# Performance work log

Measured on AMD Instinct MI355X. Metric: run time of the kernel, lower is better.

The kernel has to match this reference:

```python
import jax, jax.numpy as jnp
import numpy as np

NMUL = 1
NEARZERO = 1e-5
ROUTING_LEN = 15
N_DYN = 3
N_STATIC = 13  # layout includes parRT, parAC (present in STATIC_PARAM_NAMES but unused in the step)


def _descale(x, lb, ub):
    return lb + x * (ub - lb)


def setup_inputs() -> dict:
    key = jax.random.key(0)
    k1, k2, k3 = jax.random.split(key, 3)
    T, G = 365, 50000
    u = jax.random.uniform(k1, (T, G, 3), dtype=jnp.float32)
    prcp = u[..., 0] * 10.0                 # mm/day
    tmean = (u[..., 1] - 0.3) * 20.0        # degC, roughly [-6, 14] so snow branch is exercised
    pet = u[..., 2] * 5.0                   # mm/day
    forcing = jnp.stack([prcp, tmean, pet], axis=-1)
    dyn_raw = jax.random.uniform(k2, (T, G, N_DYN * NMUL), dtype=jnp.float32)
    static_raw = jax.random.uniform(k3, (G, N_STATIC * NMUL + 2), dtype=jnp.float32)
    return {"forcing": forcing, "dyn_raw": dyn_raw, "static_raw": static_raw}


def _hbv_forward(forcing, dyn_raw, static_raw):
    T, G, _ = forcing.shape
    dt = forcing.dtype
    # --- descale dynamic params (per-timestep): parBETA, parK0, parBETAET ---
    dyn = dyn_raw.reshape(T, G, N_DYN, NMUL)
    parBETA = _descale(dyn[:, :, 0], 1.0, 6.0)
    parK0 = _descale(dyn[:, :, 1], 0.05, 0.9)
    parBETAET = _descale(dyn[:, :, 2], 0.3, 5.0)
    # --- descale static params ---
    st = static_raw[:, :N_STATIC * NMUL].reshape(G, N_STATIC, NMUL)
    parFC = _descale(st[:, 0], 50.0, 1000.0)
    parK1 = _descale(st[:, 1], 0.01, 0.5)
    parK2 = _descale(st[:, 2], 0.001, 0.2)
    parLP = _descale(st[:, 3], 0.2, 1.0)
    parPERC = _descale(st[:, 4], 0.0, 10.0)
    parUZL = _descale(st[:, 5], 0.0, 100.0)
    parTT = _descale(st[:, 6], -2.5, 2.5)
    parCFMAX = _descale(st[:, 7], 0.5, 10.0)
    parCFR = _descale(st[:, 8], 0.0, 0.1)
    parCWH = _descale(st[:, 9], 0.0, 0.2)
    parC = _descale(st[:, 10], 0.0, 1.0)
    rout = static_raw[:, N_STATIC * NMUL:]
    rout_a = _descale(rout[:, 0], 0.0, 2.9)
    rout_b = _descale(rout[:, 1], 0.0, 6.5)

    Pm = jnp.broadcast_to(forcing[..., 0:1], (T, G, NMUL))
    Tm = jnp.broadcast_to(forcing[..., 1:2], (T, G, NMUL))
    PETm = jnp.broadcast_to(forcing[..., 2:3], (T, G, NMUL))

    def step(carry, xs):
        SNOWPACK, MELTWATER, SM, SUZ, SLZ = carry
        PRECIP, TEMP, PET, pBETA, pK0, pBETAET = xs
        is_rain = (TEMP >= parTT).astype(dt)
        RAIN = PRECIP * is_rain
        SNOW = PRECIP * (1.0 - is_rain)
        SNOWPACK = SNOWPACK + SNOW
        melt = jnp.minimum(jnp.maximum(parCFMAX * (TEMP - parTT), 0.0), SNOWPACK)
        MELTWATER = MELTWATER + melt
        SNOWPACK = SNOWPACK - melt
        refreezing = jnp.minimum(jnp.maximum(parCFR * parCFMAX * (parTT - TEMP), 0.0), MELTWATER)
        SNOWPACK = SNOWPACK + refreezing
        MELTWATER = MELTWATER - refreezing
        tosoil = jnp.maximum(MELTWATER - parCWH * SNOWPACK, 0.0)
        MELTWATER = MELTWATER - tosoil
        soil_wetness = jnp.clip((SM / parFC) ** pBETA, 0.0, 1.0)
        recharge = (RAIN + tosoil) * soil_wetness
        SM = SM + RAIN + tosoil - recharge
        excess = jnp.maximum(SM - parFC, 0.0)
        SM = SM - excess
        evapfactor = jnp.clip((SM / (parLP * parFC)) ** pBETAET, 0.0, 1.0)
        ETact = jnp.minimum(SM, PET * evapfactor)
        SM = jnp.maximum(SM - ETact, NEARZERO)
        capillary = jnp.minimum(SLZ, parC * SLZ * (1.0 - jnp.minimum(SM / parFC, 1.0)))
        SM = jnp.maximum(SM + capillary, NEARZERO)
        SLZ = jnp.maximum(SLZ - capillary, NEARZERO)
        SUZ = SUZ + recharge + excess
        PERC = jnp.minimum(SUZ, parPERC)
        SUZ = SUZ - PERC
        Q0 = pK0 * jnp.maximum(SUZ - parUZL, 0.0)
        SUZ = SUZ - Q0
        Q1 = parK1 * SUZ
        SUZ = SUZ - Q1
        SLZ = jnp.maximum(SLZ + PERC, 0.0)
        Q2 = parK2 * SLZ
        SLZ = SLZ - Q2
        return (SNOWPACK, MELTWATER, SM, SUZ, SLZ), Q0 + Q1 + Q2

    init = tuple(jnp.full((G, NMUL), 0.001, dtype=dt) for _ in range(5))
    _, Qall = jax.lax.scan(step, init, (Pm, Tm, PETm, parBETA, parK0, parBETAET))
    Qsim = Qall.mean(axis=-1)  # [T, G]: average over nmul components

    # --- gamma unit-hydrograph routing (hydroDL UH_gamma + causal conv, lenF = 15) ---
    aa = jax.nn.relu(rout_a) + 0.1      # shape param, [G]
    theta = jax.nn.relu(rout_b) + 0.5   # scale param, [G]
    t = jnp.arange(0.5, ROUTING_LEN, dtype=dt)[:, None]  # [15, 1] midpoints
    w = (t ** (aa - 1.0)) * jnp.exp(-t / theta) / (jnp.exp(jax.lax.lgamma(aa)) * theta ** aa)
    w = w / w.sum(axis=0)  # [15, G], normalized UH weights
    Qpad = jnp.pad(Qsim, ((ROUTING_LEN - 1, 0), (0, 0)))
    # causal conv: Qrout[t] = sum_k w[k] * Qsim[t-k]; fixed 15-tap loop
    Qrout = sum(w[k] * jax.lax.dynamic_slice_in_dim(Qpad, ROUTING_LEN - 1 - k, T, axis=0)
                for k in range(ROUTING_LEN))
    return Qrout  # streamflow [T, G]


def reference(forcing, dyn_raw, static_raw):
    return _hbv_forward(forcing, dyn_raw, static_raw)
```

## Files before the change

kernel.cpp:

```cpp
#include <hip/hip_runtime.h>

#define NEARZERO 1e-5f
#define RLEN 15
#define LOG2E 1.4426950408889634f

struct __attribute__((packed, aligned(4))) F3 { float x, y, z; };
static __device__ __forceinline__ F3 ld3f(const float* p) {
    return *reinterpret_cast<const F3*>(p);
}

struct Par { float FC, invFC, invLPFC, K1, K2, PERC, UZL, TT, CFMAX, CFRC, CWH, C; };

template<int PH>
__device__ __forceinline__ void finish_step(
    const Par& pr, float& SUZ, float& SLZ,
    float rxP, float k0P,
    float (&acc)[RLEN], const float (&w)[RLEN],
    float& cs, float*& outp, int G, bool guard)
{
    SUZ += rxP;
    const float PERCv = fminf(SUZ, pr.PERC);
    SUZ -= PERCv;
    const float Q0 = k0P * fmaxf(SUZ - pr.UZL, 0.0f);
    SUZ -= Q0;
    const float Q1 = pr.K1 * SUZ;
    SUZ -= Q1;
    SLZ += PERCv;
    const float Q2 = pr.K2 * SLZ;
    SLZ -= Q2;
    const float Qs = Q0 + Q1 + Q2;

    const float qr = fmaf(w[0], Qs, acc[PH]);
    acc[PH] = 0.0f;
#pragma unroll
    for (int k = 1; k < RLEN; ++k) {
        const int j = (PH + k) % RLEN;
        acc[j] = fmaf(w[k], Qs, acc[j]);
    }
    if (guard) __builtin_nontemporal_store(qr, outp);
    outp += G;
    cs = pr.C * SLZ;
}

__device__ __forceinline__ void ab_step(
    const F3& f, const F3& d3, const Par& pr,
    float& SP, float& MW, float& SM, float& SLZ,
    float cs, float& rxP, float& k0P)
{
    const float pBETA   = fmaf(d3.x, 5.0f, 1.0f);
    const float pBETAET = fmaf(d3.z, 4.7f, 0.3f);

    const float dT   = f.y - pr.TT;
    const float RAIN = (dT >= 0.0f) ? f.x : 0.0f;
    SP += f.x - RAIN;
    const float melt = __builtin_amdgcn_fmed3f(pr.CFMAX * dT, 0.0f, SP);
    MW += melt;  SP -= melt;
    const float refr = __builtin_amdgcn_fmed3f(pr.CFRC * (0.0f - dT), 0.0f, MW);
    SP += refr;  MW -= refr;
    const float tosoil = fmaxf(fmaf(-pr.CWH, SP, MW), 0.0f);
    MW -= tosoil;

    const float sw = fminf(exp2f(pBETA * __log2f(SM * pr.invFC)), 1.0f);
    const float rt = RAIN + tosoil;
    const float rc = rt * sw;
    SM = fmaf(rt, 1.0f - sw, SM);
    const float ex = fmaxf(SM - pr.FC, 0.0f);
    SM = fminf(SM, pr.FC);
    const float ef = fminf(exp2f(pBETAET * __log2f(SM * pr.invLPFC)), 1.0f);
    SM = fmaxf(SM - f.z * ef, NEARZERO);
    const float cap = cs * (1.0f - fminf(SM * pr.invFC, 1.0f));
    SM  = fmaxf(SM + cap, NEARZERO);
    SLZ = fmaxf(SLZ - cap, NEARZERO);

    rxP = rc + ex;
    k0P = fmaf(d3.y, 0.85f, 0.05f);
}

__global__ __launch_bounds__(256, 1)
void hbv_kernel(const float* __restrict__ forcing,
                const float* __restrict__ dynr,
                const float* __restrict__ statr,
                float* __restrict__ out,
                int G)
{
    const int g  = blockIdx.x * 256 + threadIdx.x;
    const int gc = (g < G) ? g : (G - 1);
    const bool guard = (g < G);

    const float* sp = statr + (size_t)gc * 15;
    Par pr;
    pr.FC    = fmaf(sp[0], 950.0f, 50.0f);
    pr.K1    = fmaf(sp[1], 0.49f, 0.01f);
    pr.K2    = fmaf(sp[2], 0.199f, 0.001f);
    const float parLP = fmaf(sp[3], 0.8f, 0.2f);
    pr.PERC  = sp[4] * 10.0f;
    pr.UZL   = sp[5] * 100.0f;
    pr.TT    = fmaf(sp[6], 5.0f, -2.5f);
    pr.CFMAX = fmaf(sp[7], 9.5f, 0.5f);
    pr.CFRC  = (sp[8] * 0.1f) * pr.CFMAX;
    pr.CWH   = sp[9] * 0.2f;
    pr.C     = sp[10];
    const float rout_a = sp[13] * 2.9f;
    const float rout_b = sp[14] * 6.5f;
    pr.invFC   = 1.0f / pr.FC;
    pr.invLPFC = 1.0f / (parLP * pr.FC);

    const float aa    = fmaxf(rout_a, 0.0f) + 0.1f;
    const float theta = fmaxf(rout_b, 0.0f) + 0.5f;
    const float am1   = aa - 1.0f;
    const float nitl2 = -LOG2E / theta;
    float w[RLEN];
    float wsum = 0.0f;
#pragma unroll
    for (int k = 0; k < RLEN; ++k) {
        const float tk = (float)k + 0.5f;
        w[k] = exp2f(am1 * __log2f(tk) + tk * nitl2);
        wsum += w[k];
    }
    const float winv = 1.0f / wsum;
#pragma unroll
    for (int k = 0; k < RLEN; ++k) w[k] *= winv;

    float SP_ = 0.001f, MW = 0.001f, SM = 0.001f, SUZ = 0.001f, SLZ = 0.001f;
    float acc[RLEN];
#pragma unroll
    for (int k = 0; k < RLEN; ++k) acc[k] = 0.0f;
    float rxP = 0.0f, k0P = 0.0f, cs = 0.0f;

    const size_t sT = (size_t)G * 3;
    const float* pF = forcing + (size_t)gc * 3;
    const float* pD = dynr    + (size_t)gc * 3;
    float* outp = out + g;

    F3 bF[5], bD[5];
    bF[0] = ld3f(pF);          bD[0] = ld3f(pD);
    bF[1] = ld3f(pF + sT);     bD[1] = ld3f(pD + sT);
    bF[2] = ld3f(pF + 2 * sT); bD[2] = ld3f(pD + 2 * sT);
    bF[3] = ld3f(pF + 3 * sT); bD[3] = ld3f(pD + 3 * sT);
    bF[4] = ld3f(pF + 4 * sT); bD[4] = ld3f(pD + 4 * sT);

    const float* rF = pF + 5 * sT;
    const float* rD = pD + 5 * sT;

    cs = pr.C * SLZ;
    {
        const F3 f_ = bF[0], d_ = bD[0];
        bF[0] = ld3f(rF); bD[0] = ld3f(rD);
        rF += sT; rD += sT;
        __builtin_amdgcn_sched_barrier(0x7);
        ab_step(f_, d_, pr, SP_, MW, SM, SLZ, cs, rxP, k0P);
    }

#define ITER(MM, FP, DP) do { \
    constexpr int PH_ = (MM) % RLEN; \
    constexpr int S_  = ((MM) + 1) % 5; \
    finish_step<PH_>(pr, SUZ, SLZ, rxP, k0P, acc, w, cs, outp, G, guard); \
    const F3 f_ = bF[S_], d_ = bD[S_]; \
    bF[S_] = ld3f(FP); bD[S_] = ld3f(DP); \
    __builtin_amdgcn_sched_barrier(0x7); \
    ab_step(f_, d_, pr, SP_, MW, SM, SLZ, cs, rxP, k0P); \
} while (0)

#define ITERADV(MM) do { ITER(MM, rF, rD); rF += sT; rD += sT; } while (0)

#define ITER_NL(MM) do { \
    constexpr int PH_ = (MM) % RLEN; \
    constexpr int S_  = ((MM) + 1) % 5; \
    finish_step<PH_>(pr, SUZ, SLZ, rxP, k0P, acc, w, cs, outp, G, guard); \
    const F3 f_ = bF[S_], d_ = bD[S_]; \
    ab_step(f_, d_, pr, SP_, MW, SM, SLZ, cs, rxP, k0P); \
} while (0)

    for (int i = 0; i < 23; ++i) {
        ITERADV(0);  ITERADV(1);  ITERADV(2);  ITERADV(3);  ITERADV(4);
        ITERADV(5);  ITERADV(6);  ITERADV(7);  ITERADV(8);  ITERADV(9);
        ITERADV(10); ITERADV(11); ITERADV(12); ITERADV(13); ITERADV(14);
    }
    ITERADV(0);  ITERADV(1);  ITERADV(2);  ITERADV(3);  ITERADV(4);
    ITERADV(5);  ITERADV(6);  ITERADV(7);  ITERADV(8);  ITERADV(9);
    ITERADV(10); ITERADV(11); ITERADV(12); ITERADV(13);
    ITER(14, pF + (size_t)364 * sT, pD + (size_t)364 * sT);
    ITER_NL(0); ITER_NL(1); ITER_NL(2); ITER_NL(3);
    finish_step<4>(pr, SUZ, SLZ, rxP, k0P, acc, w, cs, outp, G, guard);
#undef ITER_NL
#undef ITERADV
#undef ITER
}

extern "C" void kernel_launch(void* const* d_in, const int* in_sizes, int n_in,
                              void* d_out, int out_size, void* d_ws, size_t ws_size,
                              hipStream_t stream) {
    const float* forcing = (const float*)d_in[0];
    const float* dynr    = (const float*)d_in[1];
    const float* statr   = (const float*)d_in[2];
    float* out = (float*)d_out;

    const int G = in_sizes[2] / 15;
    const int block = 256;
    const int grid  = (G + block - 1) / block;
    hbv_kernel<<<grid, block, 0, stream>>>(forcing, dynr, statr, out, G);
}
```

Baseline: 99.85 us.

## Process two catchments per thread with interleaved fused timestep for ILP

Each thread now simulates two independent grid cells (g and g+half), running their HBV recurrences interleaved in one fused step so the serial dependency chains can overlap. The prefetch depth drops from 5 to 3 timesteps per cell, and addressing moves to 32-bit byte offsets from a base pointer. This halves the thread count, trading thread-level parallelism for instruction-level parallelism, and roughly doubles register use. It assumes G is even, since odd G would leave the last cell uncomputed.

```diff
diff --git a/kernel.cpp b/kernel.cpp
--- a/kernel.cpp
+++ b/kernel.cpp
@@ -5,18 +5,153 @@
 #define LOG2E 1.4426950408889634f
 
 struct __attribute__((packed, aligned(4))) F3 { float x, y, z; };
-static __device__ __forceinline__ F3 ld3f(const float* p) {
-    return *reinterpret_cast<const F3*>(p);
+static __device__ __forceinline__ F3 ldo(const char* base, unsigned voff) {
+    return *reinterpret_cast<const F3*>(base + voff);
 }
 
 struct Par { float FC, invFC, invLPFC, K1, K2, PERC, UZL, TT, CFMAX, CFRC, CWH, C; };
 
+static __device__ __forceinline__ void load_par(const float* sp, Par& pr,
+                                                float& ra, float& rb) {
+    pr.FC    = fmaf(sp[0], 950.0f, 50.0f);
+    pr.K1    = fmaf(sp[1], 0.49f, 0.01f);
+    pr.K2    = fmaf(sp[2], 0.199f, 0.001f);
+    const float parLP = fmaf(sp[3], 0.8f, 0.2f);
+    pr.PERC  = sp[4] * 10.0f;
+    pr.UZL   = sp[5] * 100.0f;
+    pr.TT    = fmaf(sp[6], 5.0f, -2.5f);
+    pr.CFMAX = fmaf(sp[7], 9.5f, 0.5f);
+    pr.CFRC  = (sp[8] * 0.1f) * pr.CFMAX;
+    pr.CWH   = sp[9] * 0.2f;
+    pr.C     = sp[10];
+    ra       = sp[13] * 2.9f;
+    rb       = sp[14] * 6.5f;
+    pr.invFC   = 1.0f / pr.FC;
+    pr.invLPFC = 1.0f / (parLP * pr.FC);
+}
+
+static __device__ __forceinline__ void make_w(float ra, float rb, float (&w)[RLEN]) {
+    const float aa    = fmaxf(ra, 0.0f) + 0.1f;
+    const float theta = fmaxf(rb, 0.0f) + 0.5f;
+    const float am1   = aa - 1.0f;
+    const float nitl2 = -LOG2E / theta;
+    float wsum = 0.0f;
+#pragma unroll
+    for (int k = 0; k < RLEN; ++k) {
+        const float tk = (float)k + 0.5f;
+        w[k] = exp2f(am1 * __log2f(tk) + tk * nitl2);
+        wsum += w[k];
+    }
+    const float winv = 1.0f / wsum;
+#pragma unroll
+    for (int k = 0; k < RLEN; ++k) w[k] *= winv;
+}
+
+__device__ __forceinline__ void ab_step(
+    const F3& f, const F3& d3, const Par& pr,
+    float& SP, float& MW, float& SM, float& SLZ,
+    float cs, float& rxP, float& k0P)
+{
+    const float dT   = f.y - pr.TT;
+    const float RAIN = (dT >= 0.0f) ? f.x : 0.0f;
+    SP += f.x - RAIN;
+    const float melt = __builtin_amdgcn_fmed3f(pr.CFMAX * dT, 0.0f, SP);
+    MW += melt;  SP -= melt;
+    const float refr = __builtin_amdgcn_fmed3f(pr.CFRC * (0.0f - dT), 0.0f, MW);
+    SP += refr;  MW -= refr;
+    const float tosoil = fmaxf(fmaf(-pr.CWH, SP, MW), 0.0f);
+    MW -= tosoil;
+    const float sw = fminf(exp2f(fmaf(d3.x, 5.0f, 1.0f) * __log2f(SM * pr.invFC)), 1.0f);
+    const float rt = RAIN + tosoil;
+    const float rc = rt * sw;
+    SM = fmaf(rt, 1.0f - sw, SM);
+    const float ex = fmaxf(SM - pr.FC, 0.0f);
+    SM = fminf(SM, pr.FC);
+    const float ef = fminf(exp2f(fmaf(d3.z, 4.7f, 0.3f) * __log2f(SM * pr.invLPFC)), 1.0f);
+    SM = fmaxf(SM - f.z * ef, NEARZERO);
+    const float cap = cs * (1.0f - fminf(SM * pr.invFC, 1.0f));
+    SM  = fmaxf(SM + cap, NEARZERO);
+    SLZ = fmaxf(SLZ - cap, NEARZERO);
+    rxP = rc + ex;
+    k0P = fmaf(d3.y, 0.85f, 0.05f);
+}
+
 template<int PH>
-__device__ __forceinline__ void finish_step(
-    const Par& pr, float& SUZ, float& SLZ,
-    float rxP, float k0P,
-    float (&acc)[RLEN], const float (&w)[RLEN],
-    float& cs, float*& outp, int G, bool guard)
+__device__ __forceinline__ void fused2(
+    const F3 fA, const F3 dA, const F3 fB, const F3 dB,
+    const Par& pA, const Par& pB,
+    float& SPa, float& MWa, float& SMa, float& SUa, float& SLa,
+    float& SPb, float& MWb, float& SMb, float& SUb, float& SLb,
+    float& rxA, float& k0A, float& rxB, float& k0B,
+    float (&accA)[RLEN], float (&accB)[RLEN],
+    const float (&wA)[RLEN], const float (&wB)[RLEN],
+    float* oA, float* oB, bool guard)
+{
+    const float t1A = __log2f(SMa * pA.invFC);
+    const float t1B = __log2f(SMb * pB.invFC);
+    const float dTA = fA.y - pA.TT;               const float dTB = fB.y - pB.TT;
+    const float RNA = (dTA >= 0.0f) ? fA.x : 0.0f;
+    const float RNB = (dTB >= 0.0f) ? fB.x : 0.0f;
+    SPa += fA.x - RNA;                            SPb += fB.x - RNB;
+    const float mlA = __builtin_amdgcn_fmed3f(pA.CFMAX * dTA, 0.0f, SPa);
+    const float mlB = __builtin_amdgcn_fmed3f(pB.CFMAX * dTB, 0.0f, SPb);
+    MWa += mlA;  SPa -= mlA;                      MWb += mlB;  SPb -= mlB;
+    const float rfA = __builtin_amdgcn_fmed3f(pA.CFRC * (0.0f - dTA), 0.0f, MWa);
+    const float rfB = __builtin_amdgcn_fmed3f(pB.CFRC * (0.0f - dTB), 0.0f, MWb);
+    SPa += rfA;  MWa -= rfA;                      SPb += rfB;  MWb -= rfB;
+    const float tsA = fmaxf(fmaf(-pA.CWH, SPa, MWa), 0.0f);
+    const float tsB = fmaxf(fmaf(-pB.CWH, SPb, MWb), 0.0f);
+    MWa -= tsA;                                   MWb -= tsB;
+    SUa += rxA;                                   SUb += rxB;
+    const float PCa = fminf(SUa, pA.PERC);        const float PCb = fminf(SUb, pB.PERC);
+    SUa -= PCa;                                   SUb -= PCb;
+    const float Q0a = k0A * fmaxf(SUa - pA.UZL, 0.0f);
+    const float Q0b = k0B * fmaxf(SUb - pB.UZL, 0.0f);
+    SUa -= Q0a;                                   SUb -= Q0b;
+    const float Q1a = pA.K1 * SUa;                const float Q1b = pB.K1 * SUb;
+    SUa -= Q1a;                                   SUb -= Q1b;
+    const float swA = fminf(exp2f(fmaf(dA.x, 5.0f, 1.0f) * t1A), 1.0f);
+    const float swB = fminf(exp2f(fmaf(dB.x, 5.0f, 1.0f) * t1B), 1.0f);
+    SLa += PCa;                                   SLb += PCb;
+    const float Q2a = pA.K2 * SLa;                const float Q2b = pB.K2 * SLb;
+    SLa -= Q2a;                                   SLb -= Q2b;
+    const float Qsa = Q0a + Q1a + Q2a;            const float Qsb = Q0b + Q1b + Q2b;
+    const float csA = pA.C * SLa;                 const float csB = pB.C * SLb;
+    const float rtA = RNA + tsA;                  const float rtB = RNB + tsB;
+    const float rcA = rtA * swA;                  const float rcB = rtB * swB;
+    SMa = fmaf(rtA, 1.0f - swA, SMa);             SMb = fmaf(rtB, 1.0f - swB, SMb);
+    const float exA = fmaxf(SMa - pA.FC, 0.0f);   const float exB = fmaxf(SMb - pB.FC, 0.0f);
+    SMa = fminf(SMa, pA.FC);                      SMb = fminf(SMb, pB.FC);
+    const float t2A = __log2f(SMa * pA.invLPFC);
+    const float t2B = __log2f(SMb * pB.invLPFC);
+    const float qrA = fmaf(wA[0], Qsa, accA[PH]);
+    const float qrB = fmaf(wB[0], Qsb, accB[PH]);
+    accA[PH] = 0.0f;                              accB[PH] = 0.0f;
+#pragma unroll
+    for (int k = 1; k < RLEN; ++k) {
+        const int j = (PH + k) % RLEN;
+        accA[j] = fmaf(wA[k], Qsa, accA[j]);
+        accB[j] = fmaf(wB[k], Qsb, accB[j]);
+    }
+    if (guard) {
+        __builtin_nontemporal_store(qrA, oA);
+        __builtin_nontemporal_store(qrB, oB);
+    }
+    const float efA = fminf(exp2f(fmaf(dA.z, 4.7f, 0.3f) * t2A), 1.0f);
+    const float efB = fminf(exp2f(fmaf(dB.z, 4.7f, 0.3f) * t2B), 1.0f);
+    SMa = fmaxf(SMa - fA.z * efA, NEARZERO);      SMb = fmaxf(SMb - fB.z * efB, NEARZERO);
+    const float cpA = csA * (1.0f - fminf(SMa * pA.invFC, 1.0f));
+    const float cpB = csB * (1.0f - fminf(SMb * pB.invFC, 1.0f));
+    SMa = fmaxf(SMa + cpA, NEARZERO);             SMb = fmaxf(SMb + cpB, NEARZERO);
+    SLa = fmaxf(SLa - cpA, NEARZERO);             SLb = fmaxf(SLb - cpB, NEARZERO);
+    rxA = rcA + exA;                              rxB = rcB + exB;
+    k0A = fmaf(dA.y, 0.85f, 0.05f);               k0B = fmaf(dB.y, 0.85f, 0.05f);
+}
+
+template<int PH>
+__device__ __forceinline__ void finish_last(
+    const Par& pr, float& SUZ, float& SLZ, float rxP, float k0P,
+    float (&acc)[RLEN], const float (&w)[RLEN], float* outp, bool guard)
 {
     SUZ += rxP;
     const float PERCv = fminf(SUZ, pr.PERC);
@@ -29,51 +164,8 @@
     const float Q2 = pr.K2 * SLZ;
     SLZ -= Q2;
     const float Qs = Q0 + Q1 + Q2;
-
     const float qr = fmaf(w[0], Qs, acc[PH]);
-    acc[PH] = 0.0f;
-#pragma unroll
-    for (int k = 1; k < RLEN; ++k) {
-        const int j = (PH + k) % RLEN;
-        acc[j] = fmaf(w[k], Qs, acc[j]);
-    }
     if (guard) __builtin_nontemporal_store(qr, outp);
-    outp += G;
-    cs = pr.C * SLZ;
-}
-
-__device__ __forceinline__ void ab_step(
-    const F3& f, const F3& d3, const Par& pr,
-    float& SP, float& MW, float& SM, float& SLZ,
-    float cs, float& rxP, float& k0P)
-{
-    const float pBETA   = fmaf(d3.x, 5.0f, 1.0f);
-    const float pBETAET = fmaf(d3.z, 4.7f, 0.3f);
-
-    const float dT   = f.y - pr.TT;
-    const float RAIN = (dT >= 0.0f) ? f.x : 0.0f;
-    SP += f.x - RAIN;
-    const float melt = __builtin_amdgcn_fmed3f(pr.CFMAX * dT, 0.0f, SP);
-    MW += melt;  SP -= melt;
-    const float refr = __builtin_amdgcn_fmed3f(pr.CFRC * (0.0f - dT), 0.0f, MW);
-    SP += refr;  MW -= refr;
-    const float tosoil = fmaxf(fmaf(-pr.CWH, SP, MW), 0.0f);
-    MW -= tosoil;
-
-    const float sw = fminf(exp2f(pBETA * __log2f(SM * pr.invFC)), 1.0f);
-    const float rt = RAIN + tosoil;
-    const float rc = rt * sw;
-    SM = fmaf(rt, 1.0f - sw, SM);
-    const float ex = fmaxf(SM - pr.FC, 0.0f);
-    SM = fminf(SM, pr.FC);
-    const float ef = fminf(exp2f(pBETAET * __log2f(SM * pr.invLPFC)), 1.0f);
-    SM = fmaxf(SM - f.z * ef, NEARZERO);
-    const float cap = cs * (1.0f - fminf(SM * pr.invFC, 1.0f));
-    SM  = fmaxf(SM + cap, NEARZERO);
-    SLZ = fmaxf(SLZ - cap, NEARZERO);
-
-    rxP = rc + ex;
-    k0P = fmaf(d3.y, 0.85f, 0.05f);
 }
 
 __global__ __launch_bounds__(256, 1)
@@ -81,108 +173,85 @@
                 const float* __restrict__ dynr,
                 const float* __restrict__ statr,
                 float* __restrict__ out,
-                int G)
-{
-    const int g  = blockIdx.x * 256 + threadIdx.x;
-    const int gc = (g < G) ? g : (G - 1);
-    const bool guard = (g < G);
-
-    const float* sp = statr + (size_t)gc * 15;
-    Par pr;
-    pr.FC    = fmaf(sp[0], 950.0f, 50.0f);
-    pr.K1    = fmaf(sp[1], 0.49f, 0.01f);
-    pr.K2    = fmaf(sp[2], 0.199f, 0.001f);
-    const float parLP = fmaf(sp[3], 0.8f, 0.2f);
-    pr.PERC  = sp[4] * 10.0f;
-    pr.UZL   = sp[5] * 100.0f;
-    pr.TT    = fmaf(sp[6], 5.0f, -2.5f);
-    pr.CFMAX = fmaf(sp[7], 9.5f, 0.5f);
-    pr.CFRC  = (sp[8] * 0.1f) * pr.CFMAX;
-    pr.CWH   = sp[9] * 0.2f;
-    pr.C     = sp[10];
-    const float rout_a = sp[13] * 2.9f;
-    const float rout_b = sp[14] * 6.5f;
-    pr.invFC   = 1.0f / pr.FC;
-    pr.invLPFC = 1.0f / (parLP * pr.FC);
-
-    const float aa    = fmaxf(rout_a, 0.0f) + 0.1f;
-    const float theta = fmaxf(rout_b, 0.0f) + 0.5f;
-    const float am1   = aa - 1.0f;
-    const float nitl2 = -LOG2E / theta;
-    float w[RLEN];
-    float wsum = 0.0f;
-#pragma unroll
-    for (int k = 0; k < RLEN; ++k) {
-        const float tk = (float)k + 0.5f;
-        w[k] = exp2f(am1 * __log2f(tk) + tk * nitl2);
-        wsum += w[k];
-    }
-    const float winv = 1.0f / wsum;
-#pragma unroll
-    for (int k = 0; k < RLEN; ++k) w[k] *= winv;
-
-    float SP_ = 0.001f, MW = 0.001f, SM = 0.001f, SUZ = 0.001f, SLZ = 0.001f;
-    float acc[RLEN];
-#pragma unroll
-    for (int k = 0; k < RLEN; ++k) acc[k] = 0.0f;
-    float rxP = 0.0f, k0P = 0.0f, cs = 0.0f;
-
-    const size_t sT = (size_t)G * 3;
-    const float* pF = forcing + (size_t)gc * 3;
-    const float* pD = dynr    + (size_t)gc * 3;
-    float* outp = out + g;
-
-    F3 bF[5], bD[5];
-    bF[0] = ld3f(pF);          bD[0] = ld3f(pD);
-    bF[1] = ld3f(pF + sT);     bD[1] = ld3f(pD + sT);
-    bF[2] = ld3f(pF + 2 * sT); bD[2] = ld3f(pD + 2 * sT);
-    bF[3] = ld3f(pF + 3 * sT); bD[3] = ld3f(pD + 3 * sT);
-    bF[4] = ld3f(pF + 4 * sT); bD[4] = ld3f(pD + 4 * sT);
-
-    const float* rF = pF + 5 * sT;
-    const float* rD = pD + 5 * sT;
-
-    cs = pr.C * SLZ;
+                int G, int half)
+{
+    const int g = blockIdx.x * 256 + threadIdx.x;
+    const bool guard = (g < half);
+    const int gA = guard ? g : (half - 1);
+    const int gB = gA + half;
+
+    Par pA, pB; float raA, rbA, raB, rbB;
+    load_par(statr + (size_t)gA * 15, pA, raA, rbA);
+    load_par(statr + (size_t)gB * 15, pB, raB, rbB);
+    float wA[RLEN], wB[RLEN];
+    make_w(raA, rbA, wA);
+    make_w(raB, rbB, wB);
+
+    float SPa = 0.001f, MWa = 0.001f, SMa = 0.001f, SUa = 0.001f, SLa = 0.001f;
+    float SPb = 0.001f, MWb = 0.001f, SMb = 0.001f, SUb = 0.001f, SLb = 0.001f;
+    float accA[RLEN], accB[RLEN];
+#pragma unroll
+    for (int k = 0; k < RLEN; ++k) { accA[k] = 0.0f; accB[k] = 0.0f; }
+    float rxA = 0.0f, k0A = 0.0f, rxB = 0.0f, k0B = 0.0f;
+
+    const char* fbase = (const char*)forcing;
+    const char* dbase = (const char*)dynr;
+    char*       obase = (char*)out;
+    const unsigned G12 = (unsigned)G * 12u;
+    const unsigned G4  = (unsigned)G * 4u;
+    const unsigned HB4 = (unsigned)half * 4u;
+    unsigned vA = (unsigned)gA * 12u;
+    unsigned vB = (unsigned)gB * 12u;
+    unsigned vO = (unsigned)g * 4u;
+
+    F3 bFA[3], bDA[3], bFB[3], bDB[3];
+#pragma unroll
+    for (int r = 0; r < 3; ++r) {
+        bFA[r] = ldo(fbase, vA); bDA[r] = ldo(dbase, vA);
+        bFB[r] = ldo(fbase, vB); bDB[r] = ldo(dbase, vB);
+        vA += G12; vB += G12;
+    }
+
     {
-        const F3 f_ = bF[0], d_ = bD[0];
-        bF[0] = ld3f(rF); bD[0] = ld3f(rD);
-        rF += sT; rD += sT;
+        const float cs0A = pA.C * SLa, cs0B = pB.C * SLb;
+        const F3 fA_ = bFA[0], dA_ = bDA[0], fB_ = bFB[0], dB_ = bDB[0];
+        bFA[0] = ldo(fbase, vA); bDA[0] = ldo(dbase, vA);
+        bFB[0] = ldo(fbase, vB); bDB[0] = ldo(dbase, vB);
+        vA += G12; vB += G12;
         __builtin_amdgcn_sched_barrier(0x7);
-        ab_step(f_, d_, pr, SP_, MW, SM, SLZ, cs, rxP, k0P);
-    }
-
-#define ITER(MM, FP, DP) do { \
+        ab_step(fA_, dA_, pA, SPa, MWa, SMa, SLa, cs0A, rxA, k0A);
+        ab_step(fB_, dB_, pB, SPb, MWb, SMb, SLb, cs0B, rxB, k0B);
+    }
+
+#define ITER(MM, VLA, VLB, DOLOAD) do { \
     constexpr int PH_ = (MM) % RLEN; \
-    constexpr int S_  = ((MM) + 1) % 5; \
-    finish_step<PH_>(pr, SUZ, SLZ, rxP, k0P, acc, w, cs, outp, G, guard); \
-    const F3 f_ = bF[S_], d_ = bD[S_]; \
-    bF[S_] = ld3f(FP); bD[S_] = ld3f(DP); \
+    constexpr int S_  = ((MM) + 1) % 3; \
+    const F3 fA_ = bFA[S_], dA_ = bDA[S_], fB_ = bFB[S_], dB_ = bDB[S_]; \
+    if (DOLOAD) { \
+        bFA[S_] = ldo(fbase, (VLA)); bDA[S_] = ldo(dbase, (VLA)); \
+        bFB[S_] = ldo(fbase, (VLB)); bDB[S_] = ldo(dbase, (VLB)); \
+    } \
     __builtin_amdgcn_sched_barrier(0x7); \
-    ab_step(f_, d_, pr, SP_, MW, SM, SLZ, cs, rxP, k0P); \
+    fused2<PH_>(fA_, dA_, fB_, dB_, pA, pB, \
+                SPa, MWa, SMa, SUa, SLa, SPb, MWb, SMb, SUb, SLb, \
+                rxA, k0A, rxB, k0B, accA, accB, wA, wB, \
+                (float*)(obase + vO), (float*)(obase + vO + HB4), guard); \
+    vO += G4; \
 } while (0)
 
-#define ITERADV(MM) do { ITER(MM, rF, rD); rF += sT; rD += sT; } while (0)
-
-#define ITER_NL(MM) do { \
-    constexpr int PH_ = (MM) % RLEN; \
-    constexpr int S_  = ((MM) + 1) % 5; \
-    finish_step<PH_>(pr, SUZ, SLZ, rxP, k0P, acc, w, cs, outp, G, guard); \
-    const F3 f_ = bF[S_], d_ = bD[S_]; \
-    ab_step(f_, d_, pr, SP_, MW, SM, SLZ, cs, rxP, k0P); \
-} while (0)
-
-    for (int i = 0; i < 23; ++i) {
+#define ITERADV(MM) do { ITER(MM, vA, vB, true); vA += G12; vB += G12; } while (0)
+
+    for (int i = 0; i < 24; ++i) {
         ITERADV(0);  ITERADV(1);  ITERADV(2);  ITERADV(3);  ITERADV(4);
         ITERADV(5);  ITERADV(6);  ITERADV(7);  ITERADV(8);  ITERADV(9);
         ITERADV(10); ITERADV(11); ITERADV(12); ITERADV(13); ITERADV(14);
     }
-    ITERADV(0);  ITERADV(1);  ITERADV(2);  ITERADV(3);  ITERADV(4);
-    ITERADV(5);  ITERADV(6);  ITERADV(7);  ITERADV(8);  ITERADV(9);
-    ITERADV(10); ITERADV(11); ITERADV(12); ITERADV(13);
-    ITER(14, pF + (size_t)364 * sT, pD + (size_t)364 * sT);
-    ITER_NL(0); ITER_NL(1); ITER_NL(2); ITER_NL(3);
-    finish_step<4>(pr, SUZ, SLZ, rxP, k0P, acc, w, cs, outp, G, guard);
-#undef ITER_NL
+    ITER(0, vA, vB, true);
+    ITER(1, 0u, 0u, false);
+    ITER(2, 0u, 0u, false);
+    ITER(3, 0u, 0u, false);
+    finish_last<4>(pA, SUa, SLa, rxA, k0A, accA, wA, (float*)(obase + vO), guard);
+    finish_last<4>(pB, SUb, SLb, rxB, k0B, accB, wB, (float*)(obase + vO + HB4), guard);
 #undef ITERADV
 #undef ITER
 }
@@ -195,8 +264,9 @@
     const float* statr   = (const float*)d_in[2];
     float* out = (float*)d_out;
 
-    const int G = in_sizes[2] / 15;
+    const int G    = in_sizes[2] / 15;
+    const int half = G / 2;
     const int block = 256;
-    const int grid  = (G + block - 1) / block;
-    hbv_kernel<<<grid, block, 0, stream>>>(forcing, dynr, statr, out, G);
-}
+    const int grid  = (half + block - 1) / block;
+    hbv_kernel<<<grid, block, 0, stream>>>(forcing, dynr, statr, out, G, half);
+}
```

Result: slower. 146.4 us (+46.7%).
